# Optimization experiments

Measured on AMD Instinct MI355X. Metric: run time of the kernel, lower is better.

## Reference

```python
import jax, jax.numpy as jnp
import numpy as np

L = 65536   # path length
D = 6       # path channels
K = 4       # signature truncation depth (max of sig_orders)


def setup_inputs() -> dict:
    key = jax.random.key(0)
    # scale keeps high-order signature terms numerically tame over 65k steps
    x = jax.random.normal(key, (L, D), dtype=jnp.float32) * 0.05
    return {"x": x}


def _signature(x):
    """Truncated path signature (levels 1..K), flattened, via Chen's relation.

    Signature of one linear segment with increment dx is exp(dx) in the
    tensor algebra: level k term = dx^{(x)k} / k!.  Full-path signature is the
    Chen (tensor-algebra) product of the per-segment exponentials, computed
    with a left-fold scan over increments.
    """
    dx = x[1:] - x[:-1]                       # (N, D) increments
    N = dx.shape[0]
    # Vectorized exp(dx) levels: E[k-1] = dx^{(x)k}/k!, flattened (N, D^k)
    E = [dx]
    for k in range(2, K + 1):
        Ek = jnp.einsum('na,nb->nab', E[-1], dx).reshape(N, -1) / k
        E.append(Ek)

    S0 = tuple(jnp.zeros((D ** (k + 1),), dtype=x.dtype) for k in range(K))

    def chen(S, e):
        # T_k = S_k + e_k + sum_{i=1}^{k-1} S_i (x) e_{k-i}   (S_0 = e_0 = 1)
        T = []
        for k in range(K):
            t = S[k] + e[k]
            for i in range(k):
                t = t + jnp.einsum('a,b->ab', S[i], e[k - 1 - i]).reshape(-1)
            T.append(t)
        return tuple(T), None

    S, _ = jax.lax.scan(chen, S0, tuple(E))
    # flatten levels 1..K: shape (D + D^2 + ... + D^K,) = (1554,)
    return jnp.concatenate(S)


def reference(x):
    return _signature(x)
```

## Files before the change

kernel.cpp:

```cpp
#include <hip/hip_runtime.h>

#define DIM 6
#define NSEG 65535
#define CH 64
#define WPB 4
#define NBLK 256

#define PSTRIDE 1568
#define PL1 0
#define PL2 8
#define PL3 48
#define PL4 264
#define NGRP 259

__device__ __forceinline__ void chen_vals(const float* __restrict__ A,
                                          const float* __restrict__ B,
                                          int g, float* v) {
    if (g == 0) {
#pragma unroll
        for (int d = 0; d < 6; ++d) v[d] = A[PL1 + d] + B[PL1 + d];
    } else if (g < 7) {
        int a = g - 1;
        float a1 = A[PL1 + a];
        const float* Ar = A + PL2 + a * 6;
        const float* Br = B + PL2 + a * 6;
#pragma unroll
        for (int d = 0; d < 6; ++d) v[d] = Ar[d] + Br[d] + a1 * B[PL1 + d];
    } else if (g < 43) {
        int ab = g - 7, a = ab / 6, b = ab - a * 6;
        float a2 = A[PL2 + ab], a1 = A[PL1 + a];
        const float* Ar = A + PL3 + ab * 6;
        const float* Br = B + PL3 + ab * 6;
        const float* B2r = B + PL2 + b * 6;
#pragma unroll
        for (int d = 0; d < 6; ++d)
            v[d] = Ar[d] + Br[d] + a2 * B[PL1 + d] + a1 * B2r[d];
    } else {
        int abc = g - 43, ab = abc / 6, cc = abc - ab * 6, a = abc / 36,
            bc = abc - a * 36;
        float a3 = A[PL3 + abc], a2 = A[PL2 + ab], a1 = A[PL1 + a];
        const float* Ar = A + PL4 + abc * 6;
        const float* Br = B + PL4 + abc * 6;
        const float* B2r = B + PL2 + cc * 6;
        const float* B3r = B + PL3 + bc * 6;
#pragma unroll
        for (int d = 0; d < 6; ++d)
            v[d] = Ar[d] + Br[d] + a3 * B[PL1 + d] + a2 * B2r[d] + a1 * B3r[d];
    }
}

__device__ __forceinline__ int grp_off_padded(int g) {
    if (g == 0) return PL1;
    if (g < 7) return PL2 + (g - 1) * 6;
    if (g < 43) return PL3 + (g - 7) * 6;
    return PL4 + (g - 43) * 6;
}
__device__ __forceinline__ int grp_off_flat(int g) {
    if (g == 0) return 0;
    if (g < 7) return 6 + (g - 1) * 6;
    if (g < 43) return 42 + (g - 7) * 6;
    return 258 + (g - 43) * 6;
}

__device__ __forceinline__ void write_final(float* out, int flat_out, int g,
                                            const float* v, int blk) {
    if (flat_out) {
        int off = grp_off_flat(g);
#pragma unroll
        for (int d = 0; d < 6; ++d) out[off + d] = v[d];
    } else {
        float* O = out + (size_t)blk * PSTRIDE;
        int off = grp_off_padded(g);
#pragma unroll
        for (int d = 0; d < 6; ++d) O[off + d] = v[d];
    }
}

__global__ __launch_bounds__(256) void sig_fold4(const float* __restrict__ x,
                                                 float* __restrict__ part) {
    __shared__ __align__(16) float dxs[WPB * CH * 8];
    __shared__ __align__(16) float P[WPB * PSTRIDE];
    __shared__ __align__(16) float Q[2 * PSTRIDE];
    const int t = threadIdx.x;
    const int w = t >> 6;
    const int lane = t & 63;
    const int c = blockIdx.x * WPB + w;
    const int j0 = c * CH;
    const int cnt = min(CH, NSEG - j0);

    float* dxw = dxs + w * (CH * 8);
    for (int f = lane; f < CH * 8; f += 64) dxw[f] = 0.f;
    __syncthreads();
    const float* xb = x + (size_t)j0 * DIM;
    for (int f = lane; f < cnt * DIM; f += 64) {
        int j = f / 6, k = f - j * 6;
        dxw[j * 8 + k] = xb[f + 6] - xb[f];
    }
    __syncthreads();

    const int ab = (lane < 36) ? lane : 35;
    const int a = ab / 6, b = ab - a * 6;
    const float* dxap = dxw + a;
    const float* dxbp = dxw + b;

    float r4[36], r3[6], r2 = 0.f, s1 = 0.f;
#pragma unroll
    for (int i = 0; i < 36; ++i) r4[i] = 0.f;
#pragma unroll
    for (int i = 0; i < 6; ++i) r3[i] = 0.f;

#pragma unroll 2
    for (int j = 0; j < CH; ++j) {
        const float4 q0 = *(const float4*)(dxw + j * 8);
        const float2 q1 = *(const float2*)(dxw + j * 8 + 4);
        const float dxv[6] = {q0.x, q0.y, q0.z, q0.w, q1.x, q1.y};
        const float dxa = dxap[j * 8];
        const float dxb = dxbp[j * 8];

        float t2 = fmaf(dxb, fmaf(dxa, (1.f / 12.f), s1 * (1.f / 3.f)), r2);
        float t2h = 0.5f * t2;
        float wv[6];
#pragma unroll
        for (int cc = 0; cc < 6; ++cc) wv[cc] = fmaf(t2h, dxv[cc], r3[cc]);
#pragma unroll
        for (int cc = 0; cc < 6; ++cc)
#pragma unroll
            for (int d = 0; d < 6; ++d)
                r4[cc * 6 + d] = fmaf(wv[cc], dxv[d], r4[cc * 6 + d]);
        float t3 = fmaf(dxa, (1.f / 3.f), s1);
        float v = fmaf(0.5f * t3, dxb, r2);
#pragma unroll
        for (int cc = 0; cc < 6; ++cc) r3[cc] = fmaf(v, dxv[cc], r3[cc]);
        r2 = fmaf(fmaf(0.5f, dxa, s1), dxb, r2);
        s1 += dxa;
    }

    if (lane < 36) {
        float* Pw = P + w * PSTRIDE;
        if (a == b) Pw[PL1 + a] = s1;
        Pw[PL2 + ab] = r2;
        float* p3 = Pw + PL3 + ab * 6;
        *(float2*)(p3 + 0) = make_float2(r3[0], r3[1]);
        *(float2*)(p3 + 2) = make_float2(r3[2], r3[3]);
        *(float2*)(p3 + 4) = make_float2(r3[4], r3[5]);
        float* p4 = Pw + PL4 + ab * 36;
#pragma unroll
        for (int i = 0; i < 9; ++i)
            *(float4*)(p4 + 4 * i) =
                make_float4(r4[4 * i], r4[4 * i + 1], r4[4 * i + 2], r4[4 * i + 3]);
    }
    __syncthreads();

    for (int idx = t; idx < 2 * NGRP; idx += 256) {
        int p = idx / NGRP, g = idx - p * NGRP;
        float v[6];
        chen_vals(P + (2 * p) * PSTRIDE, P + (2 * p + 1) * PSTRIDE, g, v);
        float* o = Q + p * PSTRIDE + grp_off_padded(g);
#pragma unroll
        for (int d = 0; d < 6; ++d) o[d] = v[d];
    }
    __syncthreads();

    for (int idx = t; idx < NGRP; idx += 256) {
        float v[6];
        chen_vals(Q, Q + PSTRIDE, idx, v);
        float* O = part + (size_t)blockIdx.x * PSTRIDE + grp_off_padded(idx);
#pragma unroll
        for (int d = 0; d < 6; ++d) O[d] = v[d];
    }
}

__global__ __launch_bounds__(256) void sig_tree_s(const float* __restrict__ in,
                                                  float* __restrict__ out,
                                                  int np0, int flat_out) {
    __shared__ __align__(16) float LIN[8 * PSTRIDE];
    __shared__ __align__(16) float W[4 * PSTRIDE];
    const int t = threadIdx.x;
    const int gs = np0 * 2;
    const float* gbase = in + (size_t)blockIdx.x * gs * PSTRIDE;

    const int nvec = gs * (PSTRIDE / 4);
    for (int f = t; f < nvec; f += 256)
        *(float4*)(LIN + 4 * f) = *(const float4*)(gbase + 4 * f);
    __syncthreads();

    float* cur = LIN;
    float* nxt = W;
    for (int np = np0;; np >>= 1) {
        for (int idx = t; idx < np * NGRP; idx += 256) {
            int p = idx / NGRP, g = idx - p * NGRP;
            float v[6];
            chen_vals(cur + (2 * p) * PSTRIDE, cur + (2 * p + 1) * PSTRIDE, g, v);
            if (np == 1) {
                write_final(out, flat_out, g, v, blockIdx.x);
            } else {
                float* o = nxt + p * PSTRIDE + grp_off_padded(g);
#pragma unroll
                for (int d = 0; d < 6; ++d) o[d] = v[d];
            }
        }
        if (np == 1) break;
        __syncthreads();
        float* tmp = cur; cur = nxt; nxt = tmp;
    }
}

extern "C" void kernel_launch(void* const* d_in, const int* in_sizes, int n_in,
                              void* d_out, int out_size, void* d_ws, size_t ws_size,
                              hipStream_t stream) {
    const float* x = (const float*)d_in[0];
    float* out = (float*)d_out;
    float* ws0 = (float*)d_ws;
    float* ws1 = ws0 + (size_t)NBLK * PSTRIDE;
    float* ws2 = ws1 + (size_t)32 * PSTRIDE;

    sig_fold4<<<NBLK, 256, 0, stream>>>(x, ws0);
    sig_tree_s<<<32, 256, 0, stream>>>(ws0, ws1, 4, 0);
    sig_tree_s<<<4, 256, 0, stream>>>(ws1, ws2, 4, 0);
    sig_tree_s<<<1, 256, 0, stream>>>(ws2, out, 2, 1);
}
```

Baseline: 92.54 us.

## Fuse fold and tree reduction into one cooperative kernel with grid syncs

Merges the per-chunk fold kernel and three tree-reduction launches into a single cooperative kernel that uses grid-wide syncs between stages. The reduction tree becomes two levels of 16-way folds instead of three levels of 8/8/4. This removes kernel launch gaps and intermediate launch overhead, at the cost of grid-sync latency and a larger shared-memory union (24 partials) that could lower occupancy. All 256 blocks must be co-resident for the cooperative launch.

```diff
diff --git a/kernel.cpp b/kernel.cpp
--- a/kernel.cpp
+++ b/kernel.cpp
@@ -1,4 +1,7 @@
 #include <hip/hip_runtime.h>
+#include <hip/hip_cooperative_groups.h>
+
+namespace cg = cooperative_groups;
 
 #define DIM 6
 #define NSEG 65535
@@ -62,137 +65,25 @@
     return 258 + (g - 43) * 6;
 }
 
-__device__ __forceinline__ void write_final(float* out, int flat_out, int g,
-                                            const float* v, int blk) {
-    if (flat_out) {
-        int off = grp_off_flat(g);
-#pragma unroll
-        for (int d = 0; d < 6; ++d) out[off + d] = v[d];
-    } else {
-        float* O = out + (size_t)blk * PSTRIDE;
-        int off = grp_off_padded(g);
-#pragma unroll
-        for (int d = 0; d < 6; ++d) O[off + d] = v[d];
-    }
-}
-
-__global__ __launch_bounds__(256) void sig_fold4(const float* __restrict__ x,
-                                                 float* __restrict__ part) {
-    __shared__ __align__(16) float dxs[WPB * CH * 8];
-    __shared__ __align__(16) float P[WPB * PSTRIDE];
-    __shared__ __align__(16) float Q[2 * PSTRIDE];
-    const int t = threadIdx.x;
-    const int w = t >> 6;
-    const int lane = t & 63;
-    const int c = blockIdx.x * WPB + w;
-    const int j0 = c * CH;
-    const int cnt = min(CH, NSEG - j0);
-
-    float* dxw = dxs + w * (CH * 8);
-    for (int f = lane; f < CH * 8; f += 64) dxw[f] = 0.f;
-    __syncthreads();
-    const float* xb = x + (size_t)j0 * DIM;
-    for (int f = lane; f < cnt * DIM; f += 64) {
-        int j = f / 6, k = f - j * 6;
-        dxw[j * 8 + k] = xb[f + 6] - xb[f];
-    }
-    __syncthreads();
-
-    const int ab = (lane < 36) ? lane : 35;
-    const int a = ab / 6, b = ab - a * 6;
-    const float* dxap = dxw + a;
-    const float* dxbp = dxw + b;
-
-    float r4[36], r3[6], r2 = 0.f, s1 = 0.f;
-#pragma unroll
-    for (int i = 0; i < 36; ++i) r4[i] = 0.f;
-#pragma unroll
-    for (int i = 0; i < 6; ++i) r3[i] = 0.f;
-
-#pragma unroll 2
-    for (int j = 0; j < CH; ++j) {
-        const float4 q0 = *(const float4*)(dxw + j * 8);
-        const float2 q1 = *(const float2*)(dxw + j * 8 + 4);
-        const float dxv[6] = {q0.x, q0.y, q0.z, q0.w, q1.x, q1.y};
-        const float dxa = dxap[j * 8];
-        const float dxb = dxbp[j * 8];
-
-        float t2 = fmaf(dxb, fmaf(dxa, (1.f / 12.f), s1 * (1.f / 3.f)), r2);
-        float t2h = 0.5f * t2;
-        float wv[6];
-#pragma unroll
-        for (int cc = 0; cc < 6; ++cc) wv[cc] = fmaf(t2h, dxv[cc], r3[cc]);
-#pragma unroll
-        for (int cc = 0; cc < 6; ++cc)
-#pragma unroll
-            for (int d = 0; d < 6; ++d)
-                r4[cc * 6 + d] = fmaf(wv[cc], dxv[d], r4[cc * 6 + d]);
-        float t3 = fmaf(dxa, (1.f / 3.f), s1);
-        float v = fmaf(0.5f * t3, dxb, r2);
-#pragma unroll
-        for (int cc = 0; cc < 6; ++cc) r3[cc] = fmaf(v, dxv[cc], r3[cc]);
-        r2 = fmaf(fmaf(0.5f, dxa, s1), dxb, r2);
-        s1 += dxa;
-    }
-
-    if (lane < 36) {
-        float* Pw = P + w * PSTRIDE;
-        if (a == b) Pw[PL1 + a] = s1;
-        Pw[PL2 + ab] = r2;
-        float* p3 = Pw + PL3 + ab * 6;
-        *(float2*)(p3 + 0) = make_float2(r3[0], r3[1]);
-        *(float2*)(p3 + 2) = make_float2(r3[2], r3[3]);
-        *(float2*)(p3 + 4) = make_float2(r3[4], r3[5]);
-        float* p4 = Pw + PL4 + ab * 36;
-#pragma unroll
-        for (int i = 0; i < 9; ++i)
-            *(float4*)(p4 + 4 * i) =
-                make_float4(r4[4 * i], r4[4 * i + 1], r4[4 * i + 2], r4[4 * i + 3]);
-    }
-    __syncthreads();
-
-    for (int idx = t; idx < 2 * NGRP; idx += 256) {
-        int p = idx / NGRP, g = idx - p * NGRP;
-        float v[6];
-        chen_vals(P + (2 * p) * PSTRIDE, P + (2 * p + 1) * PSTRIDE, g, v);
-        float* o = Q + p * PSTRIDE + grp_off_padded(g);
-#pragma unroll
-        for (int d = 0; d < 6; ++d) o[d] = v[d];
-    }
-    __syncthreads();
-
-    for (int idx = t; idx < NGRP; idx += 256) {
-        float v[6];
-        chen_vals(Q, Q + PSTRIDE, idx, v);
-        float* O = part + (size_t)blockIdx.x * PSTRIDE + grp_off_padded(idx);
-#pragma unroll
-        for (int d = 0; d < 6; ++d) O[d] = v[d];
-    }
-}
-
-__global__ __launch_bounds__(256) void sig_tree_s(const float* __restrict__ in,
-                                                  float* __restrict__ out,
-                                                  int np0, int flat_out) {
-    __shared__ __align__(16) float LIN[8 * PSTRIDE];
-    __shared__ __align__(16) float W[4 * PSTRIDE];
-    const int t = threadIdx.x;
-    const int gs = np0 * 2;
-    const float* gbase = in + (size_t)blockIdx.x * gs * PSTRIDE;
-
-    const int nvec = gs * (PSTRIDE / 4);
-    for (int f = t; f < nvec; f += 256)
-        *(float4*)(LIN + 4 * f) = *(const float4*)(gbase + 4 * f);
-    __syncthreads();
-
-    float* cur = LIN;
-    float* nxt = W;
-    for (int np = np0;; np >>= 1) {
+__device__ __forceinline__ void tree16(float* cur, float* nxt, float* out,
+                                       int flat_out, int out_blk, int t) {
+    int np = 8;
+    while (true) {
         for (int idx = t; idx < np * NGRP; idx += 256) {
             int p = idx / NGRP, g = idx - p * NGRP;
             float v[6];
             chen_vals(cur + (2 * p) * PSTRIDE, cur + (2 * p + 1) * PSTRIDE, g, v);
             if (np == 1) {
-                write_final(out, flat_out, g, v, blockIdx.x);
+                if (flat_out) {
+                    int off = grp_off_flat(g);
+#pragma unroll
+                    for (int d = 0; d < 6; ++d) out[off + d] = v[d];
+                } else {
+                    float* O = out + (size_t)out_blk * PSTRIDE;
+                    int off = grp_off_padded(g);
+#pragma unroll
+                    for (int d = 0; d < 6; ++d) O[off + d] = v[d];
+                }
             } else {
                 float* o = nxt + p * PSTRIDE + grp_off_padded(g);
 #pragma unroll
@@ -202,6 +93,132 @@
         if (np == 1) break;
         __syncthreads();
         float* tmp = cur; cur = nxt; nxt = tmp;
+        np >>= 1;
+    }
+}
+
+__global__ __launch_bounds__(256) void sig_all(const float* __restrict__ x,
+                                               float* __restrict__ ws0,
+                                               float* __restrict__ ws1,
+                                               float* __restrict__ out) {
+    __shared__ __align__(16) union SH {
+        struct { float dxs[WPB * CH * 8]; float P[WPB * PSTRIDE];
+                 float Q[2 * PSTRIDE]; } a;
+        struct { float LIN[16 * PSTRIDE]; float W[8 * PSTRIDE]; } b;
+    } sh;
+    const int t = threadIdx.x;
+
+    {
+        const int w = t >> 6;
+        const int lane = t & 63;
+        const int c = blockIdx.x * WPB + w;
+        const int j0 = c * CH;
+        const int cnt = min(CH, NSEG - j0);
+
+        float* dxw = sh.a.dxs + w * (CH * 8);
+        for (int f = lane; f < CH * 8; f += 64) dxw[f] = 0.f;
+        __syncthreads();
+        const float* xb = x + (size_t)j0 * DIM;
+        for (int f = lane; f < cnt * DIM; f += 64) {
+            int j = f / 6, k = f - j * 6;
+            dxw[j * 8 + k] = xb[f + 6] - xb[f];
+        }
+        __syncthreads();
+
+        const int ab = (lane < 36) ? lane : 35;
+        const int a = ab / 6, b = ab - a * 6;
+        const float* dxap = dxw + a;
+        const float* dxbp = dxw + b;
+
+        float r4[36], r3[6], r2 = 0.f, s1 = 0.f;
+#pragma unroll
+        for (int i = 0; i < 36; ++i) r4[i] = 0.f;
+#pragma unroll
+        for (int i = 0; i < 6; ++i) r3[i] = 0.f;
+
+#pragma unroll 2
+        for (int j = 0; j < CH; ++j) {
+            const float4 q0 = *(const float4*)(dxw + j * 8);
+            const float2 q1 = *(const float2*)(dxw + j * 8 + 4);
+            const float dxv[6] = {q0.x, q0.y, q0.z, q0.w, q1.x, q1.y};
+            const float dxa = dxap[j * 8];
+            const float dxb = dxbp[j * 8];
+
+            float t2 = fmaf(dxb, fmaf(dxa, (1.f / 12.f), s1 * (1.f / 3.f)), r2);
+            float t2h = 0.5f * t2;
+            float wv[6];
+#pragma unroll
+            for (int cc = 0; cc < 6; ++cc) wv[cc] = fmaf(t2h, dxv[cc], r3[cc]);
+#pragma unroll
+            for (int cc = 0; cc < 6; ++cc)
+#pragma unroll
+                for (int d = 0; d < 6; ++d)
+                    r4[cc * 6 + d] = fmaf(wv[cc], dxv[d], r4[cc * 6 + d]);
+            float t3 = fmaf(dxa, (1.f / 3.f), s1);
+            float v = fmaf(0.5f * t3, dxb, r2);
+#pragma unroll
+            for (int cc = 0; cc < 6; ++cc) r3[cc] = fmaf(v, dxv[cc], r3[cc]);
+            r2 = fmaf(fmaf(0.5f, dxa, s1), dxb, r2);
+            s1 += dxa;
+        }
+
+        if (lane < 36) {
+            float* Pw = sh.a.P + w * PSTRIDE;
+            if (a == b) Pw[PL1 + a] = s1;
+            Pw[PL2 + ab] = r2;
+            float* p3 = Pw + PL3 + ab * 6;
+            *(float2*)(p3 + 0) = make_float2(r3[0], r3[1]);
+            *(float2*)(p3 + 2) = make_float2(r3[2], r3[3]);
+            *(float2*)(p3 + 4) = make_float2(r3[4], r3[5]);
+            float* p4 = Pw + PL4 + ab * 36;
+#pragma unroll
+            for (int i = 0; i < 9; ++i)
+                *(float4*)(p4 + 4 * i) = make_float4(r4[4 * i], r4[4 * i + 1],
+                                                     r4[4 * i + 2], r4[4 * i + 3]);
+        }
+        __syncthreads();
+
+        for (int idx = t; idx < 2 * NGRP; idx += 256) {
+            int p = idx / NGRP, g = idx - p * NGRP;
+            float v[6];
+            chen_vals(sh.a.P + (2 * p) * PSTRIDE, sh.a.P + (2 * p + 1) * PSTRIDE,
+                      g, v);
+            float* o = sh.a.Q + p * PSTRIDE + grp_off_padded(g);
+#pragma unroll
+            for (int d = 0; d < 6; ++d) o[d] = v[d];
+        }
+        __syncthreads();
+
+        for (int idx = t; idx < NGRP; idx += 256) {
+            float v[6];
+            chen_vals(sh.a.Q, sh.a.Q + PSTRIDE, idx, v);
+            float* O = ws0 + (size_t)blockIdx.x * PSTRIDE + grp_off_padded(idx);
+#pragma unroll
+            for (int d = 0; d < 6; ++d) O[d] = v[d];
+        }
+    }
+
+    __threadfence();
+    cg::this_grid().sync();
+
+    if (blockIdx.x < 16) {
+        const float* gbase = ws0 + (size_t)blockIdx.x * 16 * PSTRIDE;
+        const int nvec = 16 * (PSTRIDE / 4);
+        for (int f = t; f < nvec; f += 256)
+            *(float4*)(sh.b.LIN + 4 * f) = *(const float4*)(gbase + 4 * f);
+        __syncthreads();
+        tree16(sh.b.LIN, sh.b.W, ws1, 0, blockIdx.x, t);
+    }
+
+    __threadfence();
+    cg::this_grid().sync();
+
+    if (blockIdx.x == 0) {
+        const int nvec = 16 * (PSTRIDE / 4);
+        for (int f = t; f < nvec; f += 256)
+            *(float4*)(sh.b.LIN + 4 * f) = *(const float4*)(ws1 + 4 * f);
+        __syncthreads();
+        tree16(sh.b.LIN, sh.b.W, out, 1, 0, t);
     }
 }
 
@@ -212,10 +229,8 @@
     float* out = (float*)d_out;
     float* ws0 = (float*)d_ws;
     float* ws1 = ws0 + (size_t)NBLK * PSTRIDE;
-    float* ws2 = ws1 + (size_t)32 * PSTRIDE;
-
-    sig_fold4<<<NBLK, 256, 0, stream>>>(x, ws0);
-    sig_tree_s<<<32, 256, 0, stream>>>(ws0, ws1, 4, 0);
-    sig_tree_s<<<4, 256, 0, stream>>>(ws1, ws2, 4, 0);
-    sig_tree_s<<<1, 256, 0, stream>>>(ws2, out, 2, 1);
-}
+
+    void* args[] = {(void*)&x, (void*)&ws0, (void*)&ws1, (void*)&out};
+    hipLaunchCooperativeKernel((void*)sig_all, dim3(NBLK), dim3(256), args, 0,
+                               stream);
+}
```

After: 214.8 us. +132.1%, slower.
